# Kernel optimization log

Hardware: AMD Instinct MI355X
Metric: run time of the kernel (lower is better)

Reference implementation:

```python
import jax, jax.numpy as jnp
import numpy as np

B, N, E, M = 512, 101, 128, 8
DK = E // M  # 16
EPS = 1e-5

def _bn(x, g, b):
    # torch BatchNorm1d in train mode on (B, E, N): per-channel stats over batch+city dims, biased var
    mu = jnp.mean(x, axis=(0, 1))
    var = jnp.mean((x - mu) ** 2, axis=(0, 1))
    return (x - mu) * jax.lax.rsqrt(var + EPS) * g + b

def setup_inputs() -> dict:
    key = jax.random.key(0)
    ks = jax.random.split(key, 24)
    sc = 1.0 / np.sqrt(E)
    inp = {
        's': jax.random.uniform(ks[0], (B, N, 2), jnp.float32),
        'd': jax.random.randint(ks[1], (B, N, 1), 0, 10),
        'e_w': jax.random.normal(ks[2], (3, E), jnp.float32) * sc,
        'e_b': jax.random.normal(ks[3], (E,), jnp.float32) * sc,
        'ep_w': jax.random.normal(ks[4], (2, E), jnp.float32) * sc,
        'ep_b': jax.random.normal(ks[5], (E,), jnp.float32) * sc,
        'Wq': jax.random.normal(ks[6], (3, E, E), jnp.float32) * sc,
        'bq': jax.random.normal(ks[7], (3, E), jnp.float32) * sc,
        'Wk': jax.random.normal(ks[8], (3, E, E), jnp.float32) * sc,
        'bk': jax.random.normal(ks[9], (3, E), jnp.float32) * sc,
        'Wv': jax.random.normal(ks[10], (3, E, E), jnp.float32) * sc,
        'bv': jax.random.normal(ks[11], (3, E), jnp.float32) * sc,
        'Wo': jax.random.normal(ks[12], (3, E, E), jnp.float32) * sc,
        'bo': jax.random.normal(ks[13], (3, E), jnp.float32) * sc,
        'Wf1': jax.random.normal(ks[14], (3, E, 4 * E), jnp.float32) * sc,
        'bf1': jax.random.normal(ks[15], (3, 4 * E), jnp.float32) * sc,
        'Wf2': jax.random.normal(ks[16], (3, 4 * E, E), jnp.float32) * sc,
        'bf2': jax.random.normal(ks[17], (3, E), jnp.float32) * sc,
        'g1': jnp.ones((3, E), jnp.float32),
        'be1': jnp.zeros((3, E), jnp.float32),
        'g2': jnp.ones((3, E), jnp.float32),
        'be2': jnp.zeros((3, E), jnp.float32),
    }
    return inp

def reference(s, d, e_w, e_b, ep_w, ep_b, Wq, bq, Wk, bk, Wv, bv, Wo, bo,
              Wf1, bf1, Wf2, bf2, g1, be1, g2, be2):
    # node embedding: cat(coords, demand) -> Linear(3,E); depot row uses Linear(2,E)
    sss = jnp.concatenate([s, d.astype(s.dtype)], axis=2)          # (B,N,3)
    node = sss @ e_w + e_b                                         # (B,N,E)
    node = node.at[:, 0, :].set(s[:, 0, :] @ ep_w + ep_b)
    x = node
    inv_sqrt_dk = 1.0 / (DK ** 0.5)
    for i in range(3):
        res = x
        q = (x @ Wq[i] + bq[i]).reshape(B, N, M, DK)
        k = (x @ Wk[i] + bk[i]).reshape(B, N, M, DK)
        v = (x @ Wv[i] + bv[i]).reshape(B, N, M, DK)
        # scores[b,i,j,h] = <q_i, k_j> per head (source does expand*mul*sum)
        scores = jnp.einsum('bihd,bjhd->bijh', q, k) * inv_sqrt_dk  # (B,N,N,M)
        a = jax.nn.softmax(scores, axis=2)                          # over keys j
        o = jnp.einsum('bijh,bjhd->bihd', a, v).reshape(B, N, E)
        x = _bn(o @ Wo[i] + bo[i] + res, g1[i], be1[i])
        ff = jax.nn.relu(x @ Wf1[i] + bf1[i]) @ Wf2[i] + bf2[i]
        x = _bn(x + ff, g2[i], be2[i])
    return x
```

## Files before the change

kernel.cpp:

```cpp
#include <hip/hip_runtime.h>
#include <hip/hip_fp16.h>
#include <stdint.h>

#define TROWS 51712
#define NCITY 101
#define BATCH 512
#define EDIM  128
#define NBH   4096

using half_t = _Float16;
typedef __attribute__((ext_vector_type(8))) _Float16 h8;
typedef __attribute__((ext_vector_type(4))) _Float16 h4;
typedef __attribute__((ext_vector_type(4))) float   f32x4;

typedef __attribute__((address_space(1))) const unsigned int gu32;
typedef __attribute__((address_space(3))) unsigned int lu32;
static __device__ __forceinline__ void async16(const void* g, const void* l) {
    __builtin_amdgcn_global_load_lds((gu32*)g, (lu32*)(uint32_t)(uintptr_t)l, 16, 0, 0);
}

static __device__ __forceinline__ int swz_col(int c, int row) {
    return (c & ~31) | ((((c >> 3) ^ (row >> 1)) & 3) << 3) | (c & 7);
}

__global__ __launch_bounds__(256)
void prep_kernel(const float* __restrict__ Wq, const float* __restrict__ Wk,
                 const float* __restrict__ Wv, const float* __restrict__ Wo,
                 const float* __restrict__ Wf1, const float* __restrict__ Wf2,
                 const float* __restrict__ bq, const float* __restrict__ bk,
                 const float* __restrict__ bv,
                 half_t* __restrict__ wqkv, half_t* __restrict__ wo,
                 half_t* __restrict__ wf1, half_t* __restrict__ wf2,
                 float* __restrict__ bqkv)
{
    const int which = blockIdx.y;
    const int gid = blockIdx.x * 256 + threadIdx.x;
    if (which <= 2) {
        if (gid >= 3 * 128 * 128) return;
        const float* src = (which == 0) ? Wq : (which == 1) ? Wk : Wv;
        int l = gid >> 14, r = gid & 16383, k = r >> 7, n = r & 127;
        wqkv[(size_t)l * 49152 + which * 16384 + n * 128 + swz_col(k, n)] = (half_t)src[gid];
    } else if (which == 3) {
        if (gid >= 3 * 128 * 128) return;
        int l = gid >> 14, r = gid & 16383, k = r >> 7, n = r & 127;
        wo[(size_t)l * 16384 + n * 128 + swz_col(k, n)] = (half_t)Wo[gid];
    } else if (which == 4) {
        if (gid >= 3 * 65536) return;
        int l = gid >> 16, u = gid & 65535;
        int j = u >> 13, kc = (u >> 11) & 3, n = (u >> 5) & 63, hp = u & 31;
        int k = kc * 32 + ((((hp >> 3) ^ (n >> 1)) & 3) << 3) + (hp & 7);
        wf1[(size_t)l * 65536 + u] = (half_t)Wf1[(size_t)(l * 128 + k) * 512 + j * 64 + n];
    } else if (which == 5) {
        if (gid >= 3 * 65536) return;
        int l = gid >> 16, u = gid & 65535;
        int j = u >> 13, kc = (u >> 12) & 1, n = (u >> 5) & 127, hp = u & 31;
        int kh = j * 64 + kc * 32 + ((((hp >> 3) ^ (n >> 1)) & 3) << 3) + (hp & 7);
        wf2[(size_t)l * 65536 + u] = (half_t)Wf2[(size_t)(l * 512 + kh) * 128 + n];
    } else {
        if (gid >= 3 * 384) return;
        int l = gid / 384, c = gid - l * 384;
        float v = (c < 128) ? bq[l * 128 + c]
                : (c < 256) ? bk[l * 128 + c - 128]
                            : bv[l * 128 + c - 256];
        bqkv[gid] = v;
    }
}

__global__ __launch_bounds__(256)
void embed_kernel(const float* __restrict__ s, const int* __restrict__ d,
                  const float* __restrict__ e_w, const float* __restrict__ e_b,
                  const float* __restrict__ ep_w, const float* __restrict__ ep_b,
                  half_t* __restrict__ xh)
{
    int gid = blockIdx.x * 256 + threadIdx.x;
    int row = gid >> 7;
    int c   = gid & 127;
    int b = row / NCITY;
    int n = row - b * NCITY;
    const float* sp = s + ((size_t)b * NCITY + n) * 2;
    float v;
    if (n == 0) {
        v = sp[0] * ep_w[c] + sp[1] * ep_w[128 + c] + ep_b[c];
    } else {
        float dv = (float)d[b * NCITY + n];
        v = sp[0] * e_w[c] + sp[1] * e_w[128 + c] + dv * e_w[256 + c] + e_b[c];
    }
    xh[gid] = (half_t)v;
}

__global__ __launch_bounds__(512, 1)
void layer_attn(const half_t* __restrict__ xsrc, const float* __restrict__ stats0,
                const float* __restrict__ g0, const float* __restrict__ be0,
                const half_t* __restrict__ wqkv, const float* __restrict__ bqkv,
                const half_t* __restrict__ wo, const float* __restrict__ bo,
                half_t* __restrict__ y16, float* __restrict__ stats)
{
    __shared__ alignas(16) half_t sO[112 * 136];
    __shared__ alignas(16) half_t sQKV[3][8][112 * 16];
    half_t* sX = sO;
    float* sBN2 = (float*)&sQKV[0][0][0];

    const int b   = blockIdx.x;
    const int tid = threadIdx.x;
    const int wave = tid >> 6, lane = tid & 63;
    const int quad = lane >> 4, l16 = lane & 15;
    const float invN = 1.0f / (float)TROWS;

    if (stats0) {
        if (tid < 128) {
            float mean = stats0[tid] * invN;
            float var  = stats0[128 + tid] * invN - mean * mean;
            float scl  = g0[tid] * rsqrtf(var + 1e-5f);
            sBN2[tid]       = scl;
            sBN2[128 + tid] = be0[tid] - mean * scl;
        }
        __syncthreads();
    }
    if (tid < 448) {
        int row = tid >> 2, q = tid & 3;
        int qs = ((q ^ (row >> 1)) & 3) << 3;
        h8 out[4];
        if (row < NCITY) {
            const half_t* src = xsrc + ((size_t)b * NCITY + row) * 128 + q * 8;
            #pragma unroll
            for (int kc = 0; kc < 4; ++kc) {
                h8 v = *(const h8*)(src + kc * 32);
                if (stats0) {
                    #pragma unroll
                    for (int r = 0; r < 8; ++r) {
                        int c = kc * 32 + q * 8 + r;
                        v[r] = (half_t)((float)v[r] * sBN2[c] + sBN2[128 + c]);
                    }
                }
                out[kc] = v;
            }
        } else {
            h8 z = {};
            out[0] = z; out[1] = z; out[2] = z; out[3] = z;
        }
        #pragma unroll
        for (int kc = 0; kc < 4; ++kc)
            *(h8*)(&sX[kc * 3584 + row * 32 + qs]) = out[kc];
    }
    __syncthreads();

    const int hn  = wave * 16 + l16;
    const int nsw = (hn >> 1) & 3;
    h8 bfr[3][4];
    float bv3[3];
    #pragma unroll
    for (int which = 0; which < 3; ++which) {
        const half_t* wrow = wqkv + which * 16384 + (size_t)hn * 128;
        #pragma unroll
        for (int kc = 0; kc < 4; ++kc)
            bfr[which][kc] = *(const h8*)(wrow + kc * 32 + (((quad ^ nsw) & 3) << 3));
        bv3[which] = bqkv[which * 128 + hn];
    }
    #pragma unroll
    for (int mi = 0; mi < 7; ++mi) {
        h8 af[4];
        #pragma unroll
        for (int kc = 0; kc < 4; ++kc) {
            int r = mi * 16 + l16;
            af[kc] = *(const h8*)(&sX[kc * 3584 + r * 32 + (((quad ^ (r >> 1)) & 3) << 3)]);
        }
        #pragma unroll
        for (int which = 0; which < 3; ++which) {
            f32x4 a = {};
            #pragma unroll
            for (int kc = 0; kc < 4; ++kc)
                a = __builtin_amdgcn_mfma_f32_16x16x32_f16(af[kc], bfr[which][kc], a, 0, 0, 0);
            half_t* dstL = &sQKV[which][wave][0];
            #pragma unroll
            for (int r = 0; r < 4; ++r) {
                int tok = mi * 16 + quad * 4 + r;
                int dsw = l16 ^ (((tok >> 2) & 1) << 3);
                dstL[tok * 16 + dsw] = (half_t)(a[r] + bv3[which]);
            }
        }
    }
    __syncthreads();

    const half_t* qb = &sQKV[0][wave][0];
    const half_t* kb = &sQKV[1][wave][0];
    const half_t* vb = &sQKV[2][wave][0];
    const int kflip = (l16 >> 2) & 1;

    const int s0 = (((quad & 1) * 2)    ) * 16 + l16;
    const int s1 = (((quad & 1) * 2) + 1) * 16 + l16;
    const bool hi2 = (quad >> 1) != 0;

    h8 kf[7];
    #pragma unroll
    for (int jt = 0; jt < 7; ++jt) {
        kf[jt] = (h8){};
        if (quad < 2)
            kf[jt] = *(const h8*)(kb + (jt * 16 + l16) * 16 + ((quad ^ kflip) << 3));
    }
    h8 vt[4];
    #pragma unroll
    for (int p = 0; p < 4; ++p)
        #pragma unroll
        for (int jj = 0; jj < 8; ++jj) {
            int tok = p * 32 + quad * 8 + jj;
            vt[p][jj] = vb[tok * 16 + (l16 ^ (((jj >> 2) & 1) << 3))];
        }

    const int ocol = hn;

    for (int it = 0; it < 7; ++it) {
        h8 qf = {};
        if (quad < 2)
            qf = *(const h8*)(qb + (it * 16 + l16) * 16 + ((quad ^ kflip) << 3));

        f32x4 S[7];
        #pragma unroll
        for (int jt = 0; jt < 7; ++jt) {
            f32x4 a = {};
            a = __builtin_amdgcn_mfma_f32_16x16x32_f16(kf[jt], qf, a, 0, 0, 0);
            S[jt] = a;
        }
        float m = -1e30f;
        #pragma unroll
        for (int jt = 0; jt < 7; ++jt)
            #pragma unroll
            for (int r = 0; r < 4; ++r) {
                int jg = jt * 16 + quad * 4 + r;
                float sv = (jg < NCITY) ? S[jt][r] * 0.25f : -1e30f;
                S[jt][r] = sv;
                m = fmaxf(m, sv);
            }
        m = fmaxf(m, __shfl_xor(m, 16));
        m = fmaxf(m, __shfl_xor(m, 32));
        float sum = 0.0f;
        #pragma unroll
        for (int jt = 0; jt < 7; ++jt)
            #pragma unroll
            for (int r = 0; r < 4; ++r) {
                float e = __expf(S[jt][r] - m);
                S[jt][r] = e;
                sum += e;
            }
        sum += __shfl_xor(sum, 16);
        sum += __shfl_xor(sum, 32);
        float inv = 1.0f / sum;
        #pragma unroll
        for (int jt = 0; jt < 7; ++jt)
            #pragma unroll
            for (int r = 0; r < 4; ++r) S[jt][r] *= inv;

        f32x4 O = {};
        #pragma unroll
        for (int p = 0; p < 4; ++p) {
            float pj[8];
            #pragma unroll
            for (int r = 0; r < 4; ++r) {
                float a0 = __shfl(S[2 * p][r],     s0);
                float b0 = __shfl(S[2 * p + 1][r], s0);
                float a1 = __shfl(S[2 * p][r],     s1);
                float b1 = __shfl(S[2 * p + 1][r], s1);
                pj[r]     = hi2 ? b0 : a0;
                pj[4 + r] = hi2 ? b1 : a1;
            }
            h8 ph;
            #pragma unroll
            for (int jj = 0; jj < 8; ++jj)
                ph[jj] = (half_t)pj[jj];
            O = __builtin_amdgcn_mfma_f32_16x16x32_f16(ph, vt[p], O, 0, 0, 0);
        }
        #pragma unroll
        for (int r = 0; r < 4; ++r) {
            int q = it * 16 + quad * 4 + r;
            int g = (ocol >> 3) ^ ((q & 8) >> 2);
            sO[q * 136 + g * 8 + (ocol & 7)] = (half_t)O[r];
        }
    }
    __syncthreads();

    h8 bfr2[4];
    {
        const half_t* wrow = wo + (size_t)ocol * 128;
        const int nsw2 = (ocol >> 1) & 3;
        #pragma unroll
        for (int kc = 0; kc < 4; ++kc)
            bfr2[kc] = *(const h8*)(wrow + kc * 32 + (((quad ^ nsw2) & 3) << 3));
    }
    f32x4 acc[7];
    #pragma unroll
    for (int mi = 0; mi < 7; ++mi) {
        acc[mi] = (f32x4){};
        int row = mi * 16 + l16;
        int swr = (row & 8) >> 2;
        #pragma unroll
        for (int kc = 0; kc < 4; ++kc) {
            h8 af = *(const h8*)(&sO[row * 136 + (((kc * 4 + quad) ^ swr) << 3)]);
            acc[mi] = __builtin_amdgcn_mfma_f32_16x16x32_f16(af, bfr2[kc], acc[mi], 0, 0, 0);
        }
    }
    float sclo = 1.0f, shfo = 0.0f;
    if (stats0) {
        float mean = stats0[ocol] * invN;
        float var  = stats0[128 + ocol] * invN - mean * mean;
        sclo = g0[ocol] * rsqrtf(var + 1e-5f);
        shfo = be0[ocol] - mean * sclo;
    }
    float bvv = bo[ocol];
    float s = 0.0f, ss = 0.0f;
    #pragma unroll
    for (int mi = 0; mi < 7; ++mi) {
        #pragma unroll
        for (int r = 0; r < 4; ++r) {
            int q = mi * 16 + quad * 4 + r;
            if (q < NCITY) {
                size_t grow = (size_t)b * NCITY + q;
                float xv = (float)xsrc[grow * 128 + ocol] * sclo + shfo;
                float o = acc[mi][r] + bvv + xv;
                y16[grow * 128 + ocol] = (half_t)o;
                s += o; ss += o * o;
            }
        }
    }
    s  += __shfl_xor(s, 16);  s  += __shfl_xor(s, 32);
    ss += __shfl_xor(ss, 16); ss += __shfl_xor(ss, 32);
    if (quad == 0) {
        atomicAdd(&stats[ocol], s);
        atomicAdd(&stats[128 + ocol], ss);
    }
}

__global__ __launch_bounds__(512, 4)
void ff_fused(half_t* __restrict__ y16, const float* __restrict__ st1,
              const float* __restrict__ g1, const float* __restrict__ be1,
              const half_t* __restrict__ w1, const half_t* __restrict__ w2,
              const float* __restrict__ bf1, const float* __restrict__ bf2,
              float* __restrict__ stats)
{
    __shared__ alignas(16) half_t sX[4][128 * 32];
    __shared__ alignas(16) half_t sW1f[8192];
    __shared__ alignas(16) half_t sW2f[8192];
    __shared__ alignas(16) half_t sH[2][128 * 32];

    const int tid  = threadIdx.x;
    const int wave = tid >> 6, lane = tid & 63;
    const int quad = lane >> 4, l16 = lane & 15;
    const int m0 = blockIdx.x * 128;
    const int wr = wave >> 1;
    const int wc = wave & 1;

    const float invN = 1.0f / (float)TROWS;
    const int so = wave * 512 + lane * 8;

    h8 rw1a = *(const h8*)(w1 + so);
    h8 rw1b = *(const h8*)(w1 + so + 4096);
    h8 rw2a = *(const h8*)(w2 + so);
    h8 rw2b = *(const h8*)(w2 + so + 4096);

    float* sBN = (float*)&sW1f[0];
    if (tid < 128) {
        float mean = st1[tid] * invN;
        float var  = st1[128 + tid] * invN - mean * mean;
        float scl  = g1[tid] * rsqrtf(var + 1e-5f);
        sBN[tid]       = scl;
        sBN[128 + tid] = be1[tid] - mean * scl;
    }
    __syncthreads();

    {
        const int row = tid >> 2;
        const int q   = tid & 3;
        const int qs  = ((q ^ (row >> 1)) & 3) << 3;
        const half_t* src = y16 + (size_t)(m0 + row) * 128 + q * 8;
        #pragma unroll
        for (int kc = 0; kc < 4; ++kc) {
            h8 v = *(const h8*)(src + kc * 32);
            h8 xv;
            #pragma unroll
            for (int r = 0; r < 8; ++r) {
                int c = kc * 32 + q * 8 + r;
                xv[r] = (half_t)((float)v[r] * sBN[c] + sBN[128 + c]);
            }
            *(h8*)(&sX[kc][row * 32 + qs]) = xv;
        }
    }

    f32x4 acc2[2][4] = {};

    for (int j = 0; j < 8; ++j) {
        asm volatile("s_waitcnt lgkmcnt(0)" ::: "memory");
        __builtin_amdgcn_s_barrier();
        __builtin_amdgcn_sched_barrier(0);
        *(h8*)(&sW1f[so])        = rw1a;
        *(h8*)(&sW1f[so + 4096]) = rw1b;
        *(h8*)(&sW2f[so])        = rw2a;
        *(h8*)(&sW2f[so + 4096]) = rw2b;
        asm volatile("s_waitcnt lgkmcnt(0)" ::: "memory");
        __builtin_amdgcn_s_barrier();
        __builtin_amdgcn_sched_barrier(0);
        if (j < 7) {
            const half_t* w1n = w1 + (size_t)(j + 1) * 8192;
            const half_t* w2n = w2 + (size_t)(j + 1) * 8192;
            rw1a = *(const h8*)(w1n + so);
            rw1b = *(const h8*)(w1n + so + 4096);
            rw2a = *(const h8*)(w2n + so);
            rw2b = *(const h8*)(w2n + so + 4096);
        }

        f32x4 acc1[2][2] = {};
        #pragma unroll
        for (int kc = 0; kc < 4; ++kc) {
            h8 af[2], bf[2];
            #pragma unroll
            for (int mi = 0; mi < 2; ++mi) {
                int r = wr * 32 + mi * 16 + l16;
                af[mi] = *(const h8*)(&sX[kc][r * 32 + (((quad ^ (r >> 1)) & 3) << 3)]);
            }
            #pragma unroll
            for (int ni = 0; ni < 2; ++ni) {
                int n = wc * 32 + ni * 16 + l16;
                bf[ni] = *(const h8*)(&sW1f[kc * 2048 + n * 32 + (((quad ^ (n >> 1)) & 3) << 3)]);
            }
            #pragma unroll
            for (int mi = 0; mi < 2; ++mi)
            #pragma unroll
            for (int ni = 0; ni < 2; ++ni)
                acc1[mi][ni] = __builtin_amdgcn_mfma_f32_16x16x32_f16(af[mi], bf[ni], acc1[mi][ni], 0, 0, 0);
        }
        #pragma unroll
        for (int ni = 0; ni < 2; ++ni) {
            int c = wc * 32 + ni * 16 + l16;
            float bvv = bf1[j * 64 + c];
            int kc2 = c >> 5, c5 = c & 31;
            #pragma unroll
            for (int mi = 0; mi < 2; ++mi)
            #pragma unroll
            for (int r = 0; r < 4; ++r) {
                int row = wr * 32 + mi * 16 + quad * 4 + r;
                float v = acc1[mi][ni][r] + bvv;
                v = v > 0.0f ? v : 0.0f;
                int hsw = (c5 & 7) | ((((c5 >> 3) ^ (row >> 1)) & 3) << 3);
                sH[kc2][row * 32 + hsw] = (half_t)v;
            }
        }
        asm volatile("s_waitcnt lgkmcnt(0)" ::: "memory");
        __builtin_amdgcn_s_barrier();
        __builtin_amdgcn_sched_barrier(0);

        #pragma unroll
        for (int kc = 0; kc < 2; ++kc) {
            h8 af[2], bf[4];
            #pragma unroll
            for (int mi = 0; mi < 2; ++mi) {
                int r = wr * 32 + mi * 16 + l16;
                af[mi] = *(const h8*)(&sH[kc][r * 32 + (((quad ^ (r >> 1)) & 3) << 3)]);
            }
            #pragma unroll
            for (int ni = 0; ni < 4; ++ni) {
                int n = wc * 64 + ni * 16 + l16;
                bf[ni] = *(const h8*)(&sW2f[kc * 4096 + n * 32 + (((quad ^ (n >> 1)) & 3) << 3)]);
            }
            #pragma unroll
            for (int mi = 0; mi < 2; ++mi)
            #pragma unroll
            for (int ni = 0; ni < 4; ++ni)
                acc2[mi][ni] = __builtin_amdgcn_mfma_f32_16x16x32_f16(af[mi], bf[ni], acc2[mi][ni], 0, 0, 0);
        }
    }

    __syncthreads();
    float* red = (float*)&sH[0][0];

    #pragma unroll
    for (int ni = 0; ni < 4; ++ni) {
        int col = wc * 64 + ni * 16 + l16;
        float bvv = bf2[col];
        int kc = col >> 5, c5 = col & 31;
        float s = 0.0f, ss = 0.0f;
        #pragma unroll
        for (int mi = 0; mi < 2; ++mi) {
            #pragma unroll
            for (int r = 0; r < 4; ++r) {
                int rowl = wr * 32 + mi * 16 + quad * 4 + r;
                int hsw = (c5 & 7) | ((((c5 >> 3) ^ (rowl >> 1)) & 3) << 3);
                float xv = (float)sX[kc][rowl * 32 + hsw];
                float o = acc2[mi][ni][r] + bvv + xv;
                y16[(size_t)(m0 + rowl) * 128 + col] = (half_t)o;
                s += o; ss += o * o;
            }
        }
        s  += __shfl_xor(s, 16);  s  += __shfl_xor(s, 32);
        ss += __shfl_xor(ss, 16); ss += __shfl_xor(ss, 32);
        if (quad == 0) {
            red[wave * 64 + ni * 16 + l16]       = s;
            red[512 + wave * 64 + ni * 16 + l16] = ss;
        }
    }
    __syncthreads();
    if (tid < 256) {
        int a   = tid >> 7;
        int col = tid & 127;
        int wcc = col >> 6, nii = (col >> 4) & 3, lx = col & 15;
        float t = 0.0f;
        #pragma unroll
        for (int w = 0; w < 4; ++w)
            t += red[a * 512 + (w * 2 + wcc) * 64 + nii * 16 + lx];
        atomicAdd(&stats[a * 128 + col], t);
    }
}

__global__ __launch_bounds__(256)
void bn_apply(const h8* __restrict__ y, const float* __restrict__ stats,
              const float* __restrict__ g, const float* __restrict__ be,
              float* __restrict__ dst32)
{
    __shared__ float sh[256];
    const int tid = threadIdx.x;
    if (tid < 128) {
        const float invN = 1.0f / (float)TROWS;
        float mean = stats[tid] * invN;
        float var  = stats[128 + tid] * invN - mean * mean;
        float inv  = rsqrtf(var + 1e-5f);
        float scl  = g[tid] * inv;
        sh[tid]       = scl;
        sh[128 + tid] = be[tid] - mean * scl;
    }
    __syncthreads();

    int gid = blockIdx.x * 256 + tid;
    int c = (gid & 15) * 8;
    h8 v = y[gid];
    float o[8];
    #pragma unroll
    for (int r = 0; r < 8; ++r)
        o[r] = (float)v[r] * sh[c + r] + sh[128 + c + r];
    f32x4 lo = { o[0], o[1], o[2], o[3] };
    f32x4 hi = { o[4], o[5], o[6], o[7] };
    ((f32x4*)dst32)[gid * 2]     = lo;
    ((f32x4*)dst32)[gid * 2 + 1] = hi;
}

extern "C" void kernel_launch(void* const* d_in, const int* in_sizes, int n_in,
                              void* d_out, int out_size, void* d_ws, size_t ws_size,
                              hipStream_t stream)
{
    const float* s    = (const float*)d_in[0];
    const int*   dd   = (const int*)d_in[1];
    const float* e_w  = (const float*)d_in[2];
    const float* e_b  = (const float*)d_in[3];
    const float* ep_w = (const float*)d_in[4];
    const float* ep_b = (const float*)d_in[5];
    const float* Wq   = (const float*)d_in[6];
    const float* bq   = (const float*)d_in[7];
    const float* Wk   = (const float*)d_in[8];
    const float* bk   = (const float*)d_in[9];
    const float* Wv   = (const float*)d_in[10];
    const float* bv   = (const float*)d_in[11];
    const float* Wo   = (const float*)d_in[12];
    const float* bo   = (const float*)d_in[13];
    const float* Wf1  = (const float*)d_in[14];
    const float* bf1  = (const float*)d_in[15];
    const float* Wf2  = (const float*)d_in[16];
    const float* bf2  = (const float*)d_in[17];
    const float* g1   = (const float*)d_in[18];
    const float* be1  = (const float*)d_in[19];
    const float* g2   = (const float*)d_in[20];
    const float* be2  = (const float*)d_in[21];

    char* ws = (char*)d_ws;
    size_t off = 0;
    auto alloc = [&](size_t bytes) -> void* {
        void* p = ws + off;
        off += (bytes + 255) & ~(size_t)255;
        return p;
    };
    half_t* y16   = (half_t*)alloc((size_t)TROWS * 128 * 2);
    half_t* xh    = (half_t*)alloc((size_t)TROWS * 128 * 2);
    half_t* wqkv  = (half_t*)alloc((size_t)3 * 384 * 128 * 2);
    half_t* wo    = (half_t*)alloc((size_t)3 * 128 * 128 * 2);
    half_t* wf1   = (half_t*)alloc((size_t)3 * 512 * 128 * 2);
    half_t* wf2   = (half_t*)alloc((size_t)3 * 128 * 512 * 2);
    float*  bqkv  = (float*) alloc((size_t)3 * 384 * 4);
    float*  stats = (float*) alloc(6 * 256 * 4);

    dim3 blk(256);

    hipMemsetAsync(stats, 0, 6 * 256 * 4, stream);

    prep_kernel<<<dim3(768, 7), blk, 0, stream>>>(Wq, Wk, Wv, Wo, Wf1, Wf2, bq, bk, bv,
                                                  wqkv, wo, wf1, wf2, bqkv);

    embed_kernel<<<dim3(TROWS * 128 / 256), blk, 0, stream>>>(s, dd, e_w, e_b, ep_w, ep_b, xh);

    for (int l = 0; l < 3; ++l) {
        float* st1 = stats + (size_t)(l * 2) * 256;
        float* st2 = stats + (size_t)(l * 2 + 1) * 256;
        const float* st0 = (l == 0) ? nullptr : stats + (size_t)((l - 1) * 2 + 1) * 256;
        const half_t* xsrc = (l == 0) ? xh : y16;
        layer_attn<<<dim3(BATCH), dim3(512), 0, stream>>>(xsrc, st0,
                                                          g2 + (l ? (l - 1) * 128 : 0),
                                                          be2 + (l ? (l - 1) * 128 : 0),
                                                          wqkv + (size_t)l * 49152,
                                                          bqkv + l * 384,
                                                          wo + (size_t)l * 16384,
                                                          bo + l * 128, y16, st1);
        ff_fused<<<dim3(404), dim3(512), 0, stream>>>(y16, st1, g1 + l * 128, be1 + l * 128,
                                                      wf1 + (size_t)l * 65536, wf2 + (size_t)l * 65536,
                                                      bf1 + l * 512, bf2 + l * 128, st2);
    }
    bn_apply<<<dim3(TROWS * 16 / 256), blk, 0, stream>>>((const h8*)y16, stats + 5 * 256,
                                                         g2 + 2 * 128, be2 + 2 * 128,
                                                         (float*)d_out);
}
```

Baseline: 379.0 us.

## Shrink attention kernel LDS footprint by aliasing buffers and raise occupancy hint

Reorganizes shared memory in the attention layer kernel into two aliased regions: Q is held in registers during the QKV projection and written over the X buffer afterwards, K and V are stored truncated to 104 rows, and the O buffer reuses the K/V region once K and V have been loaded into registers. This cuts per-block LDS use so more blocks can be resident per CU, and the launch bound is raised from 1 to 4 blocks to match. It also interleaves the Q/K/V MFMA chains. The costs are an extra barrier, extra register pressure from holding Q, and the risk that the tighter register budget causes spills.

```diff
diff --git a/kernel.cpp b/kernel.cpp
--- a/kernel.cpp
+++ b/kernel.cpp
@@ -88,17 +88,21 @@
     xh[gid] = (half_t)v;
 }
 
-__global__ __launch_bounds__(512, 1)
+__global__ __launch_bounds__(512, 4)
 void layer_attn(const half_t* __restrict__ xsrc, const float* __restrict__ stats0,
                 const float* __restrict__ g0, const float* __restrict__ be0,
                 const half_t* __restrict__ wqkv, const float* __restrict__ bqkv,
                 const half_t* __restrict__ wo, const float* __restrict__ bo,
                 half_t* __restrict__ y16, float* __restrict__ stats)
 {
-    __shared__ alignas(16) half_t sO[112 * 136];
-    __shared__ alignas(16) half_t sQKV[3][8][112 * 16];
-    half_t* sX = sO;
-    float* sBN2 = (float*)&sQKV[0][0][0];
+    __shared__ alignas(16) half_t regA[14336];
+    __shared__ alignas(16) half_t regB[26624];
+    half_t* sX = regA;
+    half_t* sQ = regA;
+    half_t* sK = regB;
+    half_t* sV = regB + 13312;
+    half_t* sO = regB;
+    float* sBN2 = (float*)regB;
 
     const int b   = blockIdx.x;
     const int tid = threadIdx.x;
@@ -156,6 +160,9 @@
             bfr[which][kc] = *(const h8*)(wrow + kc * 32 + (((quad ^ nsw) & 3) << 3));
         bv3[which] = bqkv[which * 128 + hn];
     }
+    h4 qh[7];
+    half_t* dstK = sK + wave * 1664;
+    half_t* dstV = sV + wave * 1664;
     #pragma unroll
     for (int mi = 0; mi < 7; ++mi) {
         h8 af[4];
@@ -164,48 +171,66 @@
             int r = mi * 16 + l16;
             af[kc] = *(const h8*)(&sX[kc * 3584 + r * 32 + (((quad ^ (r >> 1)) & 3) << 3)]);
         }
-        #pragma unroll
-        for (int which = 0; which < 3; ++which) {
-            f32x4 a = {};
-            #pragma unroll
-            for (int kc = 0; kc < 4; ++kc)
-                a = __builtin_amdgcn_mfma_f32_16x16x32_f16(af[kc], bfr[which][kc], a, 0, 0, 0);
-            half_t* dstL = &sQKV[which][wave][0];
+        f32x4 aq = {}, ak = {}, av = {};
+        #pragma unroll
+        for (int kc = 0; kc < 4; ++kc) {
+            aq = __builtin_amdgcn_mfma_f32_16x16x32_f16(af[kc], bfr[0][kc], aq, 0, 0, 0);
+            ak = __builtin_amdgcn_mfma_f32_16x16x32_f16(af[kc], bfr[1][kc], ak, 0, 0, 0);
+            av = __builtin_amdgcn_mfma_f32_16x16x32_f16(af[kc], bfr[2][kc], av, 0, 0, 0);
+        }
+        #pragma unroll
+        for (int r = 0; r < 4; ++r) {
+            int tok = mi * 16 + quad * 4 + r;
+            int dsw = l16 ^ (((tok >> 2) & 1) << 3);
+            qh[mi][r] = (half_t)(aq[r] + bv3[0]);
+            if (tok < 104) {
+                dstK[tok * 16 + dsw] = (half_t)(ak[r] + bv3[1]);
+                dstV[tok * 16 + dsw] = (half_t)(av[r] + bv3[2]);
+            }
+        }
+    }
+    __syncthreads();
+
+    {
+        half_t* dstQ = sQ + wave * 1792;
+        #pragma unroll
+        for (int mi = 0; mi < 7; ++mi)
             #pragma unroll
             for (int r = 0; r < 4; ++r) {
                 int tok = mi * 16 + quad * 4 + r;
                 int dsw = l16 ^ (((tok >> 2) & 1) << 3);
-                dstL[tok * 16 + dsw] = (half_t)(a[r] + bv3[which]);
-            }
-        }
-    }
-    __syncthreads();
-
-    const half_t* qb = &sQKV[0][wave][0];
-    const half_t* kb = &sQKV[1][wave][0];
-    const half_t* vb = &sQKV[2][wave][0];
+                dstQ[tok * 16 + dsw] = qh[mi][r];
+            }
+    }
+    const half_t* qb = sQ + wave * 1792;
+    const half_t* kb = sK + wave * 1664;
+    const half_t* vb = sV + wave * 1664;
     const int kflip = (l16 >> 2) & 1;
+
+    h8 kf[7];
+    #pragma unroll
+    for (int jt = 0; jt < 7; ++jt) {
+        kf[jt] = (h8){};
+        if (quad < 2) {
+            int row = jt * 16 + l16;
+            row = row < 104 ? row : 103;
+            kf[jt] = *(const h8*)(kb + row * 16 + ((quad ^ kflip) << 3));
+        }
+    }
+    h8 vt[4];
+    #pragma unroll
+    for (int p = 0; p < 4; ++p)
+        #pragma unroll
+        for (int jj = 0; jj < 8; ++jj) {
+            int tok = p * 32 + quad * 8 + jj;
+            int tokc = tok < 104 ? tok : 103;
+            vt[p][jj] = vb[tokc * 16 + (l16 ^ (((jj >> 2) & 1) << 3))];
+        }
+    __syncthreads();
 
     const int s0 = (((quad & 1) * 2)    ) * 16 + l16;
     const int s1 = (((quad & 1) * 2) + 1) * 16 + l16;
     const bool hi2 = (quad >> 1) != 0;
-
-    h8 kf[7];
-    #pragma unroll
-    for (int jt = 0; jt < 7; ++jt) {
-        kf[jt] = (h8){};
-        if (quad < 2)
-            kf[jt] = *(const h8*)(kb + (jt * 16 + l16) * 16 + ((quad ^ kflip) << 3));
-    }
-    h8 vt[4];
-    #pragma unroll
-    for (int p = 0; p < 4; ++p)
-        #pragma unroll
-        for (int jj = 0; jj < 8; ++jj) {
-            int tok = p * 32 + quad * 8 + jj;
-            vt[p][jj] = vb[tok * 16 + (l16 ^ (((jj >> 2) & 1) << 3))];
-        }
-
     const int ocol = hn;
 
     for (int it = 0; it < 7; ++it) {
```

Result: faster. 363.1 us (-4.2%).
